# Kernel tuning notes

Hardware: AMD Instinct MI355X
Metric: run time of the kernel (lower is better)

## Reference

```python
import jax, jax.numpy as jnp
import numpy as np

Q, B, N, DIM, HEADS, CODES = 4, 8, 4096, 1024, 8, 1024
DH = DIM // HEADS  # codebook_dim = 128
SCALE = DH ** -0.5


def setup_inputs() -> dict:
    key = jax.random.key(0)
    k0, k1, k2, k3 = jax.random.split(key, 4)
    return {
        "x": jax.random.normal(k0, (B, N, DIM), jnp.float32),
        "codes": jax.random.normal(k1, (Q, HEADS, CODES, DH), jnp.float32),
        "wk": jax.random.normal(k2, (Q, HEADS, DH, DH), jnp.float32) * SCALE,
        "wv": jax.random.normal(k3, (Q, HEADS, DH, DH), jnp.float32) * SCALE,
    }


def _memcodes_layer(x, codes, wk, wv):
    """One Memcodes quantizer (eval path: hard argmax).
    x: [B,N,DIM]; codes: [H,C,DH]; wk/wv: [H,DH,DH].
    Returns quantized [B,N,DIM], indices [B,H,N]."""
    b, n, _ = x.shape
    q = x.reshape(b, n, HEADS, DH).transpose(0, 2, 1, 3) * SCALE  # [b,h,n,d]
    k = jnp.einsum('hnd,hdc->hnc', codes, wk)  # [h,C,d]
    v = jnp.einsum('hnd,hdc->hnc', codes, wv)  # [h,C,d]
    logits = jnp.einsum('bhid,hjd->bhij', q, k)  # [b,h,n,C]
    idx = jnp.argmax(logits, axis=-1)  # [b,h,n]
    # one_hot(idx) @ v == gather rows of v at idx
    out = jnp.take_along_axis(v[None], idx[..., None], axis=2)  # [b,h,n,d]
    out = out.transpose(0, 2, 1, 3).reshape(b, n, DIM)
    return out, idx


def reference(x, codes, wk, wv):
    residual = x
    quantized_out = jnp.zeros_like(x)
    all_indices = []
    for i in range(Q):  # fixed small loop over quantizer layers
        quantized, idx = _memcodes_layer(residual, codes[i], wk[i], wv[i])
        residual = residual - quantized
        quantized_out = quantized_out + quantized
        all_indices.append(idx)
    return quantized_out, jnp.stack(all_indices, axis=-1)  # [B,N,DIM], [B,H,N,Q]
```

## Files before the change

### kernel.cpp

```cpp
#include <hip/hip_runtime.h>
#include <math.h>

#define QL 4
#define BB 8
#define NN 4096
#define DIMF 1024
#define HH 8
#define CC 1024
#define DH 128

#define MARGIN 4e-3f

typedef __attribute__((ext_vector_type(4))) float f32x4;
typedef __attribute__((ext_vector_type(8))) short s16x8;

__device__ __forceinline__ unsigned short f2bf(float f) {
    unsigned int u = __float_as_uint(f);
    u = u + 0x7fffu + ((u >> 16) & 1u);
    return (unsigned short)(u >> 16);
}
__device__ __forceinline__ float bf2f(unsigned short b) {
    return __uint_as_float(((unsigned int)b) << 16);
}
__device__ __forceinline__ void dma16(const void* g, void* l) {
    __builtin_amdgcn_global_load_lds(
        (const __attribute__((address_space(1))) unsigned int*)g,
        (__attribute__((address_space(3))) unsigned int*)l, 16, 0, 0);
}

#define MFMA(a, bb, c) c = __builtin_amdgcn_mfma_f32_16x16x32_bf16(a, bb, c, 0, 0, 0)

__device__ __forceinline__ void upd(float& m1, float& m2, int& mi, float v, int c) {
    m2 = fmaxf(fminf(m1, v), m2);
    if (v > m1) { m1 = v; mi = c; }
}

__global__ __launch_bounds__(128) void kv_kernel(
    const float* __restrict__ codes, const float* __restrict__ wk,
    const float* __restrict__ wv, unsigned short* __restrict__ khi,
    unsigned short* __restrict__ klo, float* __restrict__ vbuf)
{
    __shared__ float sc[8][128];
    int bid = blockIdx.x;
    int cg  = bid & 127;
    int qh  = bid >> 7;
    int t   = threadIdx.x;

    const float* cbase = codes + ((size_t)qh * CC + (size_t)cg * 8) * DH;
    #pragma unroll
    for (int i = 0; i < 8; ++i) sc[i][t] = cbase[i * DH + t];
    __syncthreads();

    const float* wkb = wk + (size_t)qh * DH * DH;
    const float* wvb = wv + (size_t)qh * DH * DH;

    float ak[8], av[8];
    #pragma unroll
    for (int i = 0; i < 8; ++i) { ak[i] = 0.f; av[i] = 0.f; }

    for (int d = 0; d < DH; ++d) {
        float a = wkb[d * DH + t];
        float b = wvb[d * DH + t];
        #pragma unroll
        for (int i = 0; i < 8; ++i) {
            ak[i] = fmaf(sc[i][d], a, ak[i]);
            av[i] = fmaf(sc[i][d], b, av[i]);
        }
    }

    size_t base = ((size_t)qh * CC + (size_t)cg * 8) * DH + t;
    #pragma unroll
    for (int i = 0; i < 8; ++i) {
        float f = ak[i];
        unsigned short hb = f2bf(f);
        unsigned short lb = f2bf(f - bf2f(hb));
        khi[base + (size_t)i * DH]  = hb;
        klo[base + (size_t)i * DH]  = lb;
        vbuf[base + (size_t)i * DH] = av[i];
    }
}

__global__ __launch_bounds__(256, 2) void fused_kernel(
    const float* __restrict__ x, const unsigned short* __restrict__ khi,
    const unsigned short* __restrict__ klo, const float* __restrict__ vbuf,
    const float* __restrict__ codes, const float* __restrict__ wk,
    const float* __restrict__ wv, float* __restrict__ out)
{
    __shared__ __align__(16) char kstage[2][16384];
    __shared__ int    chosen[128];
    __shared__ float  smax1[128];
    __shared__ int    flagged[128];
    __shared__ int    hist[QL][128];
    __shared__ int    nflag;
    __shared__ float  rbuf32[DH];
    __shared__ double rbuf64[DH];
    __shared__ double pbuf[DH];
    __shared__ int    cand[64];
    __shared__ int    ncand;
    __shared__ int    bestc;
    __shared__ double bestv;

    const int t  = threadIdx.x;
    const int w  = t >> 6;
    const int l  = t & 63;
    const int lr = l & 15;
    const int lg = l >> 4;

    const int bid = blockIdx.x;
    const int h   = bid & 7;
    const int nt  = (bid >> 3) & 31;
    const int b   = bid >> 8;
    const int n0  = nt * 128;

    const int colE  = ((l & 15) << 4) ^ ((l >> 4) << 4) ^ (((l >> 3) & 1) << 5);
    const int loffE = ((l >> 4) << 8) + colE;
    const int loffO = loffE ^ 0x40;

    s16x8 rhi[2][4], rlo[2][4];
    #pragma unroll
    for (int s = 0; s < 2; ++s) {
        const int tok = (s * 4 + w) * 16 + lr;
        const float* xp = x + ((size_t)(b * NN + n0 + tok)) * DIMF + h * DH;
        #pragma unroll
        for (int ks = 0; ks < 4; ++ks) {
            const float* p = xp + ks * 32 + lg * 8;
            float4 a = *reinterpret_cast<const float4*>(p);
            float4 c = *reinterpret_cast<const float4*>(p + 4);
            float vv[8] = {a.x, a.y, a.z, a.w, c.x, c.y, c.z, c.w};
            s16x8 hi8, lo8;
            #pragma unroll
            for (int j = 0; j < 8; ++j) {
                unsigned short hb = f2bf(vv[j]);
                unsigned short lb = f2bf(vv[j] - bf2f(hb));
                hi8[j] = (short)hb; lo8[j] = (short)lb;
            }
            rhi[s][ks] = hi8; rlo[s][ks] = lo8;
        }
    }
    if (t == 0) nflag = 0;
    __syncthreads();

    for (int q = 0; q < QL; ++q) {
        const unsigned short* khq = khi + (size_t)(q * HH + h) * CC * DH;
        const unsigned short* klq = klo + (size_t)(q * HH + h) * CC * DH;
        const float* vq = vbuf + (size_t)(q * HH + h) * CC * DH;
        const char* khc = (const char*)khq;
        const char* klc = (const char*)klq;

        auto stage4 = [&](int buf, int chunk) {
            const char* gh = khc + chunk * 8192 + w * 2048;
            const char* gl = klc + chunk * 8192 + w * 2048;
            char* lb = &kstage[buf][0] + w * 2048;
            dma16(gh + loffE, lb);
            dma16(gh + 1024 + loffO, lb + 1024);
            dma16(gl + loffE, lb + 8192);
            dma16(gl + 1024 + loffO, lb + 8192 + 1024);
        };

        float bv[2][4], b2[2][4];
        int   bi[2][4];
        #pragma unroll
        for (int s = 0; s < 2; ++s)
            #pragma unroll
            for (int r = 0; r < 4; ++r) {
                bv[s][r] = -INFINITY; b2[s][r] = -INFINITY; bi[s][r] = 0;
            }

        stage4(0, 0);

        for (int ct = 0; ct < 32; ++ct) {
            const int cur = ct & 1;
            if (ct < 31) {
                stage4(cur ^ 1, ct + 1);
                asm volatile("s_waitcnt vmcnt(4)" ::: "memory");
            } else {
                asm volatile("s_waitcnt vmcnt(0)" ::: "memory");
            }
            __builtin_amdgcn_sched_barrier(0);
            __builtin_amdgcn_s_barrier();
            __builtin_amdgcn_sched_barrier(0);

            const char* Bb = &kstage[cur][0];
            f32x4 a00 = {0.f,0.f,0.f,0.f}, a01 = {0.f,0.f,0.f,0.f};
            f32x4 a10 = {0.f,0.f,0.f,0.f}, a11 = {0.f,0.f,0.f,0.f};

            #pragma unroll
            for (int ks = 0; ks < 4; ++ks) {
                const int swz = ((ks * 64 + lg * 16) ^ ((lr & 7) << 4)) ^ ((ks >> 1) << 5);
                const char* p0 = Bb + (lr)      * 256 + swz;
                const char* p1 = Bb + (16 + lr) * 256 + swz;
                s16x8 bh0 = *reinterpret_cast<const s16x8*>(p0);
                s16x8 bh1 = *reinterpret_cast<const s16x8*>(p1);
                s16x8 bl0 = *reinterpret_cast<const s16x8*>(p0 + 8192);
                s16x8 bl1 = *reinterpret_cast<const s16x8*>(p1 + 8192);

                __builtin_amdgcn_s_setprio(1);
                MFMA(rhi[0][ks], bh0, a00); MFMA(rhi[1][ks], bh0, a10);
                MFMA(rhi[0][ks], bh1, a01); MFMA(rhi[1][ks], bh1, a11);
                MFMA(rlo[0][ks], bh0, a00); MFMA(rlo[1][ks], bh0, a10);
                MFMA(rlo[0][ks], bh1, a01); MFMA(rlo[1][ks], bh1, a11);
                MFMA(rhi[0][ks], bl0, a00); MFMA(rhi[1][ks], bl0, a10);
                MFMA(rhi[0][ks], bl1, a01); MFMA(rhi[1][ks], bl1, a11);
                __builtin_amdgcn_s_setprio(0);
            }

            {
                const int cb = ct * 32 + lr;
                #pragma unroll
                for (int r = 0; r < 4; ++r) {
                    upd(bv[0][r], b2[0][r], bi[0][r], a00[r], cb);
                    upd(bv[0][r], b2[0][r], bi[0][r], a01[r], cb + 16);
                    upd(bv[1][r], b2[1][r], bi[1][r], a10[r], cb);
                    upd(bv[1][r], b2[1][r], bi[1][r], a11[r], cb + 16);
                }
            }

            __builtin_amdgcn_sched_barrier(0);
            __builtin_amdgcn_s_barrier();
            __builtin_amdgcn_sched_barrier(0);
        }

        #pragma unroll
        for (int s = 0; s < 2; ++s) {
            #pragma unroll
            for (int r = 0; r < 4; ++r) {
                float m = bv[s][r]; float m2 = b2[s][r]; int mi = bi[s][r];
                #pragma unroll
                for (int off = 1; off <= 8; off <<= 1) {
                    float ov = __shfl_xor(m, off);
                    int   oi = __shfl_xor(mi, off);
                    float o2 = __shfl_xor(m2, off);
                    float nm2 = fmaxf(fmaxf(m2, o2), fminf(m, ov));
                    if (ov > m || (ov == m && oi < mi)) { m = ov; mi = oi; }
                    m2 = nm2;
                }
                if (lr == 0) {
                    int tok = (s * 4 + w) * 16 + lg * 4 + r;
                    chosen[tok] = mi; smax1[tok] = m;
                    int fl = (m - m2 < MARGIN) ? 1 : 0;
                    flagged[tok] = fl;
                    if (fl) atomicAdd(&nflag, 1);
                }
            }
        }
        __syncthreads();

        int nf = nflag;
        if (nf) {
            for (int tok = 0; tok < 128; ++tok) {
                if (!flagged[tok]) continue;
                if (t == 0) { ncand = 0; bestc = 0x7fffffff; bestv = -1e300; }
                if (t < DH) {
                    double r = (double)x[((size_t)(b * NN + n0 + tok)) * DIMF + h * DH + t];
                    for (int qq = 0; qq < q; ++qq) {
                        int c = hist[qq][tok];
                        const float* crow = codes + ((size_t)(qq * HH + h) * CC + c) * DH;
                        const float* wcol = wv + (size_t)(qq * HH + h) * DH * DH + t;
                        double acc = 0.0;
                        for (int dd = 0; dd < DH; ++dd)
                            acc += (double)crow[dd] * (double)wcol[(size_t)dd * DH];
                        r -= acc;
                    }
                    rbuf64[t] = r;
                    rbuf32[t] = (float)r;
                }
                __syncthreads();
                float thr = smax1[tok] - MARGIN;
                #pragma unroll
                for (int cc4 = 0; cc4 < 4; ++cc4) {
                    int c = t * 4 + cc4;
                    const unsigned short* kh = khq + (size_t)c * DH;
                    const unsigned short* kl = klq + (size_t)c * DH;
                    float acc = 0.f;
                    for (int d = 0; d < DH; ++d)
                        acc = fmaf(bf2f(kh[d]) + bf2f(kl[d]), rbuf32[d], acc);
                    if (acc >= thr) {
                        int p = atomicAdd(&ncand, 1);
                        if (p < 64) cand[p] = c;
                    }
                }
                __syncthreads();
                int nc = ncand; if (nc > 64) nc = 64;
                for (int ci = 0; ci < nc; ++ci) {
                    int c = cand[ci];
                    if (t < DH) {
                        const float* crow = codes + ((size_t)(q * HH + h) * CC + c) * DH;
                        const float* wcol = wk + (size_t)(q * HH + h) * DH * DH + t;
                        double acc = 0.0;
                        for (int dd = 0; dd < DH; ++dd)
                            acc += (double)crow[dd] * (double)wcol[(size_t)dd * DH];
                        pbuf[t] = acc * rbuf64[t];
                    }
                    __syncthreads();
                    if (t == 0) {
                        double sm = 0.0;
                        for (int dd = 0; dd < DH; ++dd) sm += pbuf[dd];
                        if (sm > bestv || (sm == bestv && c < bestc)) { bestv = sm; bestc = c; }
                    }
                    __syncthreads();
                }
                if (t == 0) chosen[tok] = bestc;
                __syncthreads();
            }
        }

        if (t < 128) hist[q][t] = chosen[t];
        if (t == 0) nflag = 0;

        #pragma unroll
        for (int s = 0; s < 2; ++s) {
            const int tok = (s * 4 + w) * 16 + lr;
            const float* vrow = vq + (size_t)chosen[tok] * DH;
            #pragma unroll
            for (int ks = 0; ks < 4; ++ks) {
                const float* p = vrow + ks * 32 + lg * 8;
                float4 a = *reinterpret_cast<const float4*>(p);
                float4 c = *reinterpret_cast<const float4*>(p + 4);
                float vv[8] = {a.x, a.y, a.z, a.w, c.x, c.y, c.z, c.w};
                s16x8 hi8 = rhi[s][ks], lo8 = rlo[s][ks], nh, nl;
                #pragma unroll
                for (int j = 0; j < 8; ++j) {
                    float f = bf2f((unsigned short)hi8[j]) +
                              bf2f((unsigned short)lo8[j]) - vv[j];
                    unsigned short hb = f2bf(f);
                    nh[j] = (short)hb;
                    nl[j] = (short)f2bf(f - bf2f(hb));
                }
                rhi[s][ks] = nh; rlo[s][ks] = nl;
            }
        }
        __syncthreads();
    }

    #pragma unroll
    for (int s = 0; s < 2; ++s) {
        const int tok = (s * 4 + w) * 16 + lr;
        const float* xp = x + ((size_t)(b * NN + n0 + tok)) * DIMF + h * DH;
        float* op = out + ((size_t)(b * NN + n0 + tok)) * DIMF + h * DH;
        #pragma unroll
        for (int ks = 0; ks < 4; ++ks) {
            const float* p = xp + ks * 32 + lg * 8;
            float4 a = *reinterpret_cast<const float4*>(p);
            float4 c = *reinterpret_cast<const float4*>(p + 4);
            s16x8 hi8 = rhi[s][ks], lo8 = rlo[s][ks];
            float4 o0, o1;
            o0.x = a.x - (bf2f((unsigned short)hi8[0]) + bf2f((unsigned short)lo8[0]));
            o0.y = a.y - (bf2f((unsigned short)hi8[1]) + bf2f((unsigned short)lo8[1]));
            o0.z = a.z - (bf2f((unsigned short)hi8[2]) + bf2f((unsigned short)lo8[2]));
            o0.w = a.w - (bf2f((unsigned short)hi8[3]) + bf2f((unsigned short)lo8[3]));
            o1.x = c.x - (bf2f((unsigned short)hi8[4]) + bf2f((unsigned short)lo8[4]));
            o1.y = c.y - (bf2f((unsigned short)hi8[5]) + bf2f((unsigned short)lo8[5]));
            o1.z = c.z - (bf2f((unsigned short)hi8[6]) + bf2f((unsigned short)lo8[6]));
            o1.w = c.w - (bf2f((unsigned short)hi8[7]) + bf2f((unsigned short)lo8[7]));
            *reinterpret_cast<float4*>(op + ks * 32 + lg * 8)     = o0;
            *reinterpret_cast<float4*>(op + ks * 32 + lg * 8 + 4) = o1;
        }
    }

    __syncthreads();
    if (t < 128) {
        float4 iv;
        iv.x = (float)hist[0][t];
        iv.y = (float)hist[1][t];
        iv.z = (float)hist[2][t];
        iv.w = (float)hist[3][t];
        float* ip = out + (size_t)BB * NN * DIMF +
                    (((size_t)(b * HH + h) * NN) + n0 + t) * QL;
        *reinterpret_cast<float4*>(ip) = iv;
    }
}

extern "C" void kernel_launch(void* const* d_in, const int* in_sizes, int n_in,
                              void* d_out, int out_size, void* d_ws, size_t ws_size,
                              hipStream_t stream) {
    const float* x     = (const float*)d_in[0];
    const float* codes = (const float*)d_in[1];
    const float* wk    = (const float*)d_in[2];
    const float* wv    = (const float*)d_in[3];
    float* out  = (float*)d_out;

    float* vbuf = (float*)d_ws;
    unsigned short* khi = (unsigned short*)(vbuf + (size_t)QL * HH * CC * DH);
    unsigned short* klo = khi + (size_t)QL * HH * CC * DH;

    kv_kernel<<<QL * HH * CC / 8, 128, 0, stream>>>(codes, wk, wv, khi, klo, vbuf);
    fused_kernel<<<BB * HH * (NN / 128), 256, 0, stream>>>(x, khi, klo, vbuf,
                                                           codes, wk, wv, out);
}
```

Before: 1.114 ms.

## Prepack K into MFMA fragment layout and load directly from global

The kv kernel now writes the bf16 hi/lo split of K in a fragment-ordered layout, 16 codes per 8KB tile, so each lane's MFMA B operand is one contiguous 16-byte load. The fused kernel drops the double-buffered LDS staging, DMA and block barriers, and reads fragments straight from global/L2 with 16-code tiles. Launch bounds change to one block per SM. This removes LDS traffic and synchronisation but depends on cache latency hiding through unrolling, and each wave now loads K independently, which raises L2 traffic.

Result: slower. 2.149 ms (+92.9%).

```diff
diff --git a/kernel.cpp b/kernel.cpp
--- a/kernel.cpp
+++ b/kernel.cpp
@@ -22,11 +22,6 @@
 __device__ __forceinline__ float bf2f(unsigned short b) {
     return __uint_as_float(((unsigned int)b) << 16);
 }
-__device__ __forceinline__ void dma16(const void* g, void* l) {
-    __builtin_amdgcn_global_load_lds(
-        (const __attribute__((address_space(1))) unsigned int*)g,
-        (__attribute__((address_space(3))) unsigned int*)l, 16, 0, 0);
-}
 
 #define MFMA(a, bb, c) c = __builtin_amdgcn_mfma_f32_16x16x32_bf16(a, bb, c, 0, 0, 0)
 
@@ -37,56 +32,85 @@
 
 __global__ __launch_bounds__(128) void kv_kernel(
     const float* __restrict__ codes, const float* __restrict__ wk,
-    const float* __restrict__ wv, unsigned short* __restrict__ khi,
-    unsigned short* __restrict__ klo, float* __restrict__ vbuf)
+    const float* __restrict__ wv, char* __restrict__ kf,
+    float* __restrict__ vbuf)
 {
-    __shared__ float sc[8][128];
-    int bid = blockIdx.x;
-    int cg  = bid & 127;
-    int qh  = bid >> 7;
-    int t   = threadIdx.x;
-
-    const float* cbase = codes + ((size_t)qh * CC + (size_t)cg * 8) * DH;
-    #pragma unroll
-    for (int i = 0; i < 8; ++i) sc[i][t] = cbase[i * DH + t];
+    __shared__ float sc[16][128];
+    __shared__ float kst[16][128];
+    __shared__ float vst[16][128];
+
+    const int bid   = blockIdx.x;
+    const int qh    = bid >> 6;
+    const int ctile = bid & 63;
+    const int t     = threadIdx.x;
+
+    const float* cbase = codes + ((size_t)qh * CC + (size_t)ctile * 16) * DH;
+    #pragma unroll
+    for (int i = 0; i < 16; ++i) sc[i][t] = cbase[i * DH + t];
     __syncthreads();
 
     const float* wkb = wk + (size_t)qh * DH * DH;
     const float* wvb = wv + (size_t)qh * DH * DH;
 
-    float ak[8], av[8];
-    #pragma unroll
-    for (int i = 0; i < 8; ++i) { ak[i] = 0.f; av[i] = 0.f; }
+    float ak[16], av[16];
+    #pragma unroll
+    for (int i = 0; i < 16; ++i) { ak[i] = 0.f; av[i] = 0.f; }
 
     for (int d = 0; d < DH; ++d) {
         float a = wkb[d * DH + t];
         float b = wvb[d * DH + t];
         #pragma unroll
-        for (int i = 0; i < 8; ++i) {
+        for (int i = 0; i < 16; ++i) {
             ak[i] = fmaf(sc[i][d], a, ak[i]);
             av[i] = fmaf(sc[i][d], b, av[i]);
         }
     }
-
-    size_t base = ((size_t)qh * CC + (size_t)cg * 8) * DH + t;
-    #pragma unroll
-    for (int i = 0; i < 8; ++i) {
-        float f = ak[i];
-        unsigned short hb = f2bf(f);
-        unsigned short lb = f2bf(f - bf2f(hb));
-        khi[base + (size_t)i * DH]  = hb;
-        klo[base + (size_t)i * DH]  = lb;
-        vbuf[base + (size_t)i * DH] = av[i];
-    }
-}
-
-__global__ __launch_bounds__(256, 2) void fused_kernel(
-    const float* __restrict__ x, const unsigned short* __restrict__ khi,
-    const unsigned short* __restrict__ klo, const float* __restrict__ vbuf,
-    const float* __restrict__ codes, const float* __restrict__ wk,
-    const float* __restrict__ wv, float* __restrict__ out)
+    #pragma unroll
+    for (int i = 0; i < 16; ++i) { kst[i][t] = ak[i]; vst[i][t] = av[i]; }
+    __syncthreads();
+
+    char* kfo = kf + ((size_t)qh * 64 + ctile) * 8192;
+    #pragma unroll
+    for (int half = 0; half < 2; ++half) {
+        int cid = t + half * 128;
+        int ks  = cid >> 6;
+        int ln  = cid & 63;
+        int lr2 = ln & 15;
+        int lg2 = ln >> 4;
+        s16x8 h8, l8;
+        #pragma unroll
+        for (int j = 0; j < 8; ++j) {
+            float f = kst[lr2][ks * 32 + lg2 * 8 + j];
+            unsigned short hb = f2bf(f);
+            h8[j] = (short)hb;
+            l8[j] = (short)f2bf(f - bf2f(hb));
+        }
+        char* pb = kfo + ks * 2048 + ln * 16;
+        *reinterpret_cast<s16x8*>(pb)        = h8;
+        *reinterpret_cast<s16x8*>(pb + 1024) = l8;
+    }
+
+    #pragma unroll
+    for (int r = 0; r < 4; ++r) {
+        int i   = t + r * 128;
+        int row = i >> 5;
+        int c4  = i & 31;
+        float4 v4;
+        v4.x = vst[row][c4 * 4 + 0];
+        v4.y = vst[row][c4 * 4 + 1];
+        v4.z = vst[row][c4 * 4 + 2];
+        v4.w = vst[row][c4 * 4 + 3];
+        *reinterpret_cast<float4*>(
+            vbuf + ((size_t)qh * CC + (size_t)ctile * 16 + row) * DH + c4 * 4) = v4;
+    }
+}
+
+__global__ __launch_bounds__(256, 1) void fused_kernel(
+    const float* __restrict__ x, const char* __restrict__ kf,
+    const float* __restrict__ vbuf, const float* __restrict__ codes,
+    const float* __restrict__ wk, const float* __restrict__ wv,
+    float* __restrict__ out)
 {
-    __shared__ __align__(16) char kstage[2][16384];
     __shared__ int    chosen[128];
     __shared__ float  smax1[128];
     __shared__ int    flagged[128];
@@ -112,10 +136,6 @@
     const int b   = bid >> 8;
     const int n0  = nt * 128;
 
-    const int colE  = ((l & 15) << 4) ^ ((l >> 4) << 4) ^ (((l >> 3) & 1) << 5);
-    const int loffE = ((l >> 4) << 8) + colE;
-    const int loffO = loffE ^ 0x40;
-
     s16x8 rhi[2][4], rlo[2][4];
     #pragma unroll
     for (int s = 0; s < 2; ++s) {
@@ -141,21 +161,8 @@
     __syncthreads();
 
     for (int q = 0; q < QL; ++q) {
-        const unsigned short* khq = khi + (size_t)(q * HH + h) * CC * DH;
-        const unsigned short* klq = klo + (size_t)(q * HH + h) * CC * DH;
-        const float* vq = vbuf + (size_t)(q * HH + h) * CC * DH;
-        const char* khc = (const char*)khq;
-        const char* klc = (const char*)klq;
-
-        auto stage4 = [&](int buf, int chunk) {
-            const char* gh = khc + chunk * 8192 + w * 2048;
-            const char* gl = klc + chunk * 8192 + w * 2048;
-            char* lb = &kstage[buf][0] + w * 2048;
-            dma16(gh + loffE, lb);
-            dma16(gh + 1024 + loffO, lb + 1024);
-            dma16(gl + loffE, lb + 8192);
-            dma16(gl + 1024 + loffO, lb + 8192 + 1024);
-        };
+        const char*  kfc = kf + (size_t)(q * HH + h) * 524288;
+        const float* vq  = vbuf + (size_t)(q * HH + h) * CC * DH;
 
         float bv[2][4], b2[2][4];
         int   bi[2][4];
@@ -166,58 +173,41 @@
                 bv[s][r] = -INFINITY; b2[s][r] = -INFINITY; bi[s][r] = 0;
             }
 
-        stage4(0, 0);
-
-        for (int ct = 0; ct < 32; ++ct) {
-            const int cur = ct & 1;
-            if (ct < 31) {
-                stage4(cur ^ 1, ct + 1);
-                asm volatile("s_waitcnt vmcnt(4)" ::: "memory");
-            } else {
-                asm volatile("s_waitcnt vmcnt(0)" ::: "memory");
-            }
-            __builtin_amdgcn_sched_barrier(0);
-            __builtin_amdgcn_s_barrier();
-            __builtin_amdgcn_sched_barrier(0);
-
-            const char* Bb = &kstage[cur][0];
-            f32x4 a00 = {0.f,0.f,0.f,0.f}, a01 = {0.f,0.f,0.f,0.f};
-            f32x4 a10 = {0.f,0.f,0.f,0.f}, a11 = {0.f,0.f,0.f,0.f};
-
-            #pragma unroll
-            for (int ks = 0; ks < 4; ++ks) {
-                const int swz = ((ks * 64 + lg * 16) ^ ((lr & 7) << 4)) ^ ((ks >> 1) << 5);
-                const char* p0 = Bb + (lr)      * 256 + swz;
-                const char* p1 = Bb + (16 + lr) * 256 + swz;
-                s16x8 bh0 = *reinterpret_cast<const s16x8*>(p0);
-                s16x8 bh1 = *reinterpret_cast<const s16x8*>(p1);
-                s16x8 bl0 = *reinterpret_cast<const s16x8*>(p0 + 8192);
-                s16x8 bl1 = *reinterpret_cast<const s16x8*>(p1 + 8192);
-
-                __builtin_amdgcn_s_setprio(1);
-                MFMA(rhi[0][ks], bh0, a00); MFMA(rhi[1][ks], bh0, a10);
-                MFMA(rhi[0][ks], bh1, a01); MFMA(rhi[1][ks], bh1, a11);
-                MFMA(rlo[0][ks], bh0, a00); MFMA(rlo[1][ks], bh0, a10);
-                MFMA(rlo[0][ks], bh1, a01); MFMA(rlo[1][ks], bh1, a11);
-                MFMA(rhi[0][ks], bl0, a00); MFMA(rhi[1][ks], bl0, a10);
-                MFMA(rhi[0][ks], bl1, a01); MFMA(rhi[1][ks], bl1, a11);
-                __builtin_amdgcn_s_setprio(0);
-            }
-
-            {
-                const int cb = ct * 32 + lr;
-                #pragma unroll
-                for (int r = 0; r < 4; ++r) {
-                    upd(bv[0][r], b2[0][r], bi[0][r], a00[r], cb);
-                    upd(bv[0][r], b2[0][r], bi[0][r], a01[r], cb + 16);
-                    upd(bv[1][r], b2[1][r], bi[1][r], a10[r], cb);
-                    upd(bv[1][r], b2[1][r], bi[1][r], a11[r], cb + 16);
-                }
-            }
-
-            __builtin_amdgcn_sched_barrier(0);
-            __builtin_amdgcn_s_barrier();
-            __builtin_amdgcn_sched_barrier(0);
+        #pragma unroll 2
+        for (int ctile = 0; ctile < 64; ++ctile) {
+            const char* pf = kfc + (size_t)ctile * 8192 + (size_t)l * 16;
+            s16x8 bh0 = *reinterpret_cast<const s16x8*>(pf);
+            s16x8 bl0 = *reinterpret_cast<const s16x8*>(pf + 1024);
+            s16x8 bh1 = *reinterpret_cast<const s16x8*>(pf + 2048);
+            s16x8 bl1 = *reinterpret_cast<const s16x8*>(pf + 3072);
+            s16x8 bh2 = *reinterpret_cast<const s16x8*>(pf + 4096);
+            s16x8 bl2 = *reinterpret_cast<const s16x8*>(pf + 5120);
+            s16x8 bh3 = *reinterpret_cast<const s16x8*>(pf + 6144);
+            s16x8 bl3 = *reinterpret_cast<const s16x8*>(pf + 7168);
+
+            f32x4 a0 = {0.f,0.f,0.f,0.f}, a1 = {0.f,0.f,0.f,0.f};
+
+            __builtin_amdgcn_s_setprio(1);
+            MFMA(rhi[0][0], bh0, a0); MFMA(rhi[1][0], bh0, a1);
+            MFMA(rlo[0][0], bh0, a0); MFMA(rlo[1][0], bh0, a1);
+            MFMA(rhi[0][0], bl0, a0); MFMA(rhi[1][0], bl0, a1);
+            MFMA(rhi[0][1], bh1, a0); MFMA(rhi[1][1], bh1, a1);
+            MFMA(rlo[0][1], bh1, a0); MFMA(rlo[1][1], bh1, a1);
+            MFMA(rhi[0][1], bl1, a0); MFMA(rhi[1][1], bl1, a1);
+            MFMA(rhi[0][2], bh2, a0); MFMA(rhi[1][2], bh2, a1);
+            MFMA(rlo[0][2], bh2, a0); MFMA(rlo[1][2], bh2, a1);
+            MFMA(rhi[0][2], bl2, a0); MFMA(rhi[1][2], bl2, a1);
+            MFMA(rhi[0][3], bh3, a0); MFMA(rhi[1][3], bh3, a1);
+            MFMA(rlo[0][3], bh3, a0); MFMA(rlo[1][3], bh3, a1);
+            MFMA(rhi[0][3], bl3, a0); MFMA(rhi[1][3], bl3, a1);
+            __builtin_amdgcn_s_setprio(0);
+
+            const int cb = ctile * 16 + lr;
+            #pragma unroll
+            for (int r = 0; r < 4; ++r) {
+                upd(bv[0][r], b2[0][r], bi[0][r], a0[r], cb);
+                upd(bv[1][r], b2[1][r], bi[1][r], a1[r], cb);
+            }
         }
 
         #pragma unroll
@@ -269,11 +259,16 @@
                 #pragma unroll
                 for (int cc4 = 0; cc4 < 4; ++cc4) {
                     int c = t * 4 + cc4;
-                    const unsigned short* kh = khq + (size_t)c * DH;
-                    const unsigned short* kl = klq + (size_t)c * DH;
+                    int lrC = c & 15, ctC = c >> 4;
+                    const char* pb = kfc + (size_t)ctC * 8192;
                     float acc = 0.f;
-                    for (int d = 0; d < DH; ++d)
-                        acc = fmaf(bf2f(kh[d]) + bf2f(kl[d]), rbuf32[d], acc);
+                    for (int d = 0; d < DH; ++d) {
+                        int ksD = d >> 5, lgD = (d >> 3) & 3, jD = d & 7;
+                        int off = ksD * 2048 + (lgD * 16 + lrC) * 16 + jD * 2;
+                        unsigned short hb = *reinterpret_cast<const unsigned short*>(pb + off);
+                        unsigned short lb = *reinterpret_cast<const unsigned short*>(pb + off + 1024);
+                        acc = fmaf(bf2f(hb) + bf2f(lb), rbuf32[d], acc);
+                    }
                     if (acc >= thr) {
                         int p = atomicAdd(&ncand, 1);
                         if (p < 64) cand[p] = c;
@@ -380,10 +375,9 @@
     float* out  = (float*)d_out;
 
     float* vbuf = (float*)d_ws;
-    unsigned short* khi = (unsigned short*)(vbuf + (size_t)QL * HH * CC * DH);
-    unsigned short* klo = khi + (size_t)QL * HH * CC * DH;
-
-    kv_kernel<<<QL * HH * CC / 8, 128, 0, stream>>>(codes, wk, wv, khi, klo, vbuf);
-    fused_kernel<<<BB * HH * (NN / 128), 256, 0, stream>>>(x, khi, klo, vbuf,
+    char*  kf   = (char*)(vbuf + (size_t)QL * HH * CC * DH);
+
+    kv_kernel<<<2048, 128, 0, stream>>>(codes, wk, wv, kf, vbuf);
+    fused_kernel<<<BB * HH * (NN / 128), 256, 0, stream>>>(x, kf, vbuf,
                                                            codes, wk, wv, out);
 }
```

## Triple-buffer codebook staging and interleave DMA segments with MFMA sub-steps

Applied to the files above, without the earlier changes.

Moves the K-codebook LDS staging from a double buffer to a triple buffer with prefetch distance two. The four DMA segments for chunk ct+2 are issued one per MFMA sub-step, with a workgroup barrier after each sub-step instead of two barriers per chunk. The aim is to hide global-to-LDS latency behind the bf16 split-precision MFMAs and spread memory issue across the tile. In exchange it uses more LDS, which may affect the 2-blocks-per-CU occupancy, and adds more frequent barriers.

Measured after the change: 1.135 ms. No clear change (+1.9%).

```diff
diff --git a/kernel.cpp b/kernel.cpp
--- a/kernel.cpp
+++ b/kernel.cpp
@@ -29,6 +29,9 @@
 }
 
 #define MFMA(a, bb, c) c = __builtin_amdgcn_mfma_f32_16x16x32_bf16(a, bb, c, 0, 0, 0)
+#define SBAR()  do { __builtin_amdgcn_sched_barrier(0); \
+                     __builtin_amdgcn_s_barrier();      \
+                     __builtin_amdgcn_sched_barrier(0); } while (0)
 
 __device__ __forceinline__ void upd(float& m1, float& m2, int& mi, float v, int c) {
     m2 = fmaxf(fminf(m1, v), m2);
@@ -86,7 +89,7 @@
     const float* __restrict__ codes, const float* __restrict__ wk,
     const float* __restrict__ wv, float* __restrict__ out)
 {
-    __shared__ __align__(16) char kstage[2][16384];
+    __shared__ __align__(16) char kstage[3][16384];
     __shared__ int    chosen[128];
     __shared__ float  smax1[128];
     __shared__ int    flagged[128];
@@ -147,14 +150,12 @@
         const char* khc = (const char*)khq;
         const char* klc = (const char*)klq;
 
-        auto stage4 = [&](int buf, int chunk) {
-            const char* gh = khc + chunk * 8192 + w * 2048;
-            const char* gl = klc + chunk * 8192 + w * 2048;
+        auto stage_seg = [&](int buf, int chunk, int seg) {
             char* lb = &kstage[buf][0] + w * 2048;
-            dma16(gh + loffE, lb);
-            dma16(gh + 1024 + loffO, lb + 1024);
-            dma16(gl + loffE, lb + 8192);
-            dma16(gl + 1024 + loffO, lb + 8192 + 1024);
+            if (seg == 0)      dma16(khc + chunk * 8192 + w * 2048 + loffE,        lb);
+            else if (seg == 1) dma16(khc + chunk * 8192 + w * 2048 + 1024 + loffO, lb + 1024);
+            else if (seg == 2) dma16(klc + chunk * 8192 + w * 2048 + loffE,        lb + 8192);
+            else               dma16(klc + chunk * 8192 + w * 2048 + 1024 + loffO, lb + 8192 + 1024);
         };
 
         float bv[2][4], b2[2][4];
@@ -166,27 +167,25 @@
                 bv[s][r] = -INFINITY; b2[s][r] = -INFINITY; bi[s][r] = 0;
             }
 
-        stage4(0, 0);
+        #pragma unroll
+        for (int seg = 0; seg < 4; ++seg) stage_seg(0, 0, seg);
+        #pragma unroll
+        for (int seg = 0; seg < 4; ++seg) stage_seg(1, 1, seg);
+        asm volatile("s_waitcnt vmcnt(4)" ::: "memory");
+        SBAR();
 
         for (int ct = 0; ct < 32; ++ct) {
-            const int cur = ct & 1;
-            if (ct < 31) {
-                stage4(cur ^ 1, ct + 1);
-                asm volatile("s_waitcnt vmcnt(4)" ::: "memory");
-            } else {
-                asm volatile("s_waitcnt vmcnt(0)" ::: "memory");
-            }
-            __builtin_amdgcn_sched_barrier(0);
-            __builtin_amdgcn_s_barrier();
-            __builtin_amdgcn_sched_barrier(0);
-
+            const int cur = ct % 3;
+            const int nxt = (ct + 2) % 3;
+            const bool pf = (ct + 2) < 32;
             const char* Bb = &kstage[cur][0];
+
             f32x4 a00 = {0.f,0.f,0.f,0.f}, a01 = {0.f,0.f,0.f,0.f};
             f32x4 a10 = {0.f,0.f,0.f,0.f}, a11 = {0.f,0.f,0.f,0.f};
 
             #pragma unroll
-            for (int ks = 0; ks < 4; ++ks) {
-                const int swz = ((ks * 64 + lg * 16) ^ ((lr & 7) << 4)) ^ ((ks >> 1) << 5);
+            for (int p = 0; p < 4; ++p) {
+                const int swz = ((p * 64 + lg * 16) ^ ((lr & 7) << 4)) ^ ((p >> 1) << 5);
                 const char* p0 = Bb + (lr)      * 256 + swz;
                 const char* p1 = Bb + (16 + lr) * 256 + swz;
                 s16x8 bh0 = *reinterpret_cast<const s16x8*>(p0);
@@ -194,30 +193,34 @@
                 s16x8 bl0 = *reinterpret_cast<const s16x8*>(p0 + 8192);
                 s16x8 bl1 = *reinterpret_cast<const s16x8*>(p1 + 8192);
 
+                if (pf) stage_seg(nxt, ct + 2, p);
+
+                SBAR();
+
                 __builtin_amdgcn_s_setprio(1);
-                MFMA(rhi[0][ks], bh0, a00); MFMA(rhi[1][ks], bh0, a10);
-                MFMA(rhi[0][ks], bh1, a01); MFMA(rhi[1][ks], bh1, a11);
-                MFMA(rlo[0][ks], bh0, a00); MFMA(rlo[1][ks], bh0, a10);
-                MFMA(rlo[0][ks], bh1, a01); MFMA(rlo[1][ks], bh1, a11);
-                MFMA(rhi[0][ks], bl0, a00); MFMA(rhi[1][ks], bl0, a10);
-                MFMA(rhi[0][ks], bl1, a01); MFMA(rhi[1][ks], bl1, a11);
+                MFMA(rhi[0][p], bh0, a00); MFMA(rhi[1][p], bh0, a10);
+                MFMA(rhi[0][p], bh1, a01); MFMA(rhi[1][p], bh1, a11);
+                MFMA(rlo[0][p], bh0, a00); MFMA(rlo[1][p], bh0, a10);
+                MFMA(rlo[0][p], bh1, a01); MFMA(rlo[1][p], bh1, a11);
+                MFMA(rhi[0][p], bl0, a00); MFMA(rhi[1][p], bl0, a10);
+                MFMA(rhi[0][p], bl1, a01); MFMA(rhi[1][p], bl1, a11);
                 __builtin_amdgcn_s_setprio(0);
-            }
-
-            {
-                const int cb = ct * 32 + lr;
-                #pragma unroll
-                for (int r = 0; r < 4; ++r) {
-                    upd(bv[0][r], b2[0][r], bi[0][r], a00[r], cb);
-                    upd(bv[0][r], b2[0][r], bi[0][r], a01[r], cb + 16);
-                    upd(bv[1][r], b2[1][r], bi[1][r], a10[r], cb);
-                    upd(bv[1][r], b2[1][r], bi[1][r], a11[r], cb + 16);
-                }
-            }
-
-            __builtin_amdgcn_sched_barrier(0);
-            __builtin_amdgcn_s_barrier();
-            __builtin_amdgcn_sched_barrier(0);
+
+                if (p == 3) {
+                    if (pf)            asm volatile("s_waitcnt vmcnt(4)" ::: "memory");
+                    else if (ct == 30) asm volatile("s_waitcnt vmcnt(0)" ::: "memory");
+                }
+                SBAR();
+            }
+
+            const int cb = ct * 32 + lr;
+            #pragma unroll
+            for (int r = 0; r < 4; ++r) {
+                upd(bv[0][r], b2[0][r], bi[0][r], a00[r], cb);
+                upd(bv[0][r], b2[0][r], bi[0][r], a01[r], cb + 16);
+                upd(bv[1][r], b2[1][r], bi[1][r], a10[r], cb);
+                upd(bv[1][r], b2[1][r], bi[1][r], a11[r], cb + 16);
+            }
         }
 
         #pragma unroll
```
